# Kernel tuning notes

Hardware: AMD Instinct MI355X
Metric: run time of the kernel (lower is better)

The kernel has to match this reference:

```python
import jax, jax.numpy as jnp
import numpy as np

RADIUS = 5
KS = 2 * RADIUS + 1  # 11
SIGMA_X2 = 4.0 ** 2  # 16
SIGMA_I2 = 10.0 ** 2  # 100


def _patches(x):
    """x: [N,1,H,W] -> [N, H*W, KS, KS] zero-padded sliding windows (torch Unfold semantics)."""
    N, _, H, W = x.shape
    p = jax.lax.conv_general_dilated_patches(
        x, (KS, KS), (1, 1), [(RADIUS, RADIUS), (RADIUS, RADIUS)]
    )  # [N, KS*KS, H, W], channel dim ordered (kh, kw)
    return p.reshape(N, KS, KS, H * W).transpose(0, 3, 1, 2)


def _distance_map(dtype):
    d = (jnp.arange(KS, dtype=dtype) - RADIUS) ** 2
    return jnp.exp(-(d[:, None] + d[None, :]) / SIGMA_X2)  # [KS, KS]


def setup_inputs() -> dict:
    key = jax.random.key(0)
    k1, k2 = jax.random.split(key)
    images = jax.random.uniform(k1, (8, 1, 224, 224), dtype=jnp.float32)
    labels = jax.random.uniform(k2, (8, 4, 224, 224), dtype=jnp.float32)
    return {"images": images, "labels": labels}


def reference(images, labels):
    B, _, H, W = images.shape
    K = labels.shape[1]
    HW = H * W

    img = images * 255.0
    regions = _patches(img)                                   # [B,HW,KS,KS]
    mask = _patches(jnp.ones((1, 1, H, W), img.dtype))        # [1,HW,KS,KS], 0 on padding
    dist_map = _distance_map(img.dtype)                       # [KS,KS]

    i_f = img.reshape(B, HW)[:, :, None, None]                # center pixel intensity
    weights = dist_map * jnp.exp(-(regions - i_f) ** 2 / SIGMA_I2) * mask  # [B,HW,KS,KS]

    # class-prob patches for all classes at once
    P = _patches(labels.reshape(B * K, 1, H, W)).reshape(B, K, HW, KS, KS)

    num = jnp.einsum('bnij,bknij->bkn', weights, P)           # sum_j w_ij * p_j
    den = weights.sum(axis=(2, 3))                            # [B,HW], sum_j w_ij
    p_f = labels.reshape(B, K, HW)

    ratio = jnp.einsum('bkn,bkn->bk', p_f, num) / jnp.einsum('bkn,bn->bk', p_f, den)
    # per-class L1Loss(ratio, 0) = mean over batch of |ratio|; summed over classes
    ratio_sum = jnp.abs(ratio).mean(axis=0).sum()
    return K - ratio_sum
```

## Files before the change

kernel.cpp:

```cpp
#include <hip/hip_runtime.h>
#include <hip/hip_bf16.h>

typedef float f2 __attribute__((ext_vector_type(2)));
typedef float f4 __attribute__((ext_vector_type(4)));

constexpr int Hh = 224, Ww = 224, Bb = 8, Kc = 4, RAD = 5;

constexpr int TX = 32;
constexpr int TILEH = 8;
constexpr int SW = TX + 2 * RAD;
constexpr int SH = TILEH + 2 * RAD;
constexpr int SSTR = SW + 1;
constexpr int GXD = Ww / TX;
constexpr int GYD = Hh / TILEH;
constexpr int PB = GXD * GYD;

constexpr float LOG2E = 1.44269504f;
constexpr float KI  = -0.01f * LOG2E;
constexpr float DSC = -0.0625f * LOG2E;

static __device__ inline f4 splat4(float x) { return (f4){x, x, x, x}; }

__global__ __launch_bounds__(256, 6) void ncut_main(const float* __restrict__ images,
                                                    const float* __restrict__ labels,
                                                    float* __restrict__ acc) {
    __shared__ float simg[SH * SSTR];
    __shared__ f4    slab[SH * SSTR];
    __shared__ float red[4][8];

    const int b   = blockIdx.z;
    const int x0  = blockIdx.x * TX;
    const int y0  = blockIdx.y * TILEH;
    const int tid = threadIdx.x;

    const float* imgb = images + (size_t)b * (Hh * Ww);
    const float* labb = labels + (size_t)b * (Kc * Hh * Ww);

    for (int idx = tid; idx < SH * SSTR; idx += 256) {
        const int lx = idx % SSTR, ly = idx / SSTR;
        const int gx = x0 - RAD + lx, gy = y0 - RAD + ly;
        float iv = 1e19f;
        f4 lv = (f4){0.f, 0.f, 0.f, 0.f};
        if (lx < SW && gx >= 0 && gx < Ww && gy >= 0 && gy < Hh) {
            const int g = gy * Ww + gx;
            iv = imgb[g] * 255.0f;
            lv = (f4){labb[g], labb[Hh * Ww + g], labb[2 * Hh * Ww + g], labb[3 * Hh * Ww + g]};
        }
        simg[idx] = iv;
        slab[idx] = lv;
    }
    __syncthreads();

    const int tx   = tid & 31;
    const int ty   = (tid >> 5) & 3;
    const int half = tid >> 7;
    const int r0   = 2 * ty;

    const float c0 = simg[(r0 + RAD) * SSTR + tx + RAD];
    const float c1 = simg[(r0 + RAD + 1) * SSTR + tx + RAD];

    f4 num0 = splat4(0.f), num1 = splat4(0.f);
    f2 den0 = (f2){0.f, 0.f}, den1 = (f2){0.f, 0.f};

#pragma unroll
    for (int r = 0; r < 6; ++r) {
        const int dr = half * 6 + r;
        const int rowoff = (r0 + dr) * SSTR + tx;
        const int   di0 = dr - 5,        di1 = dr - 6;
        const float fd0 = (float)(di0 * di0), fd1 = (float)(di1 * di1);
        const float dyw0 = (fd0 <= 25.f) ? __builtin_amdgcn_exp2f(fd0 * DSC) : 0.f;
        const float dyw1 = (fd1 <= 25.f) ? __builtin_amdgcn_exp2f(fd1 * DSC) : 0.f;
#pragma unroll
        for (int i = 0; i < 6; ++i) {
            const f2 v  = (f2){simg[rowoff + 2 * i], simg[rowoff + 2 * i + 1]};
            const f4 p0 = slab[rowoff + 2 * i];
            const f4 p1 = slab[rowoff + 2 * i + 1];
            const f2 dxt = (f2){(float)((2 * i - 5) * (2 * i - 5)) * DSC,
                                (float)((2 * i - 4) * (2 * i - 4)) * DSC};
            {
                const f2 d = v - c0;
                const f2 t = __builtin_elementwise_fma(d * KI, d, dxt);
                const float w0 = __builtin_amdgcn_exp2f(t.x) * dyw0;
                const float w1 = __builtin_amdgcn_exp2f(t.y) * dyw0;
                den0 += (f2){w0, w1};
                num0 = __builtin_elementwise_fma(splat4(w0), p0, num0);
                num0 = __builtin_elementwise_fma(splat4(w1), p1, num0);
            }
            {
                const f2 d = v - c1;
                const f2 t = __builtin_elementwise_fma(d * KI, d, dxt);
                const float w0 = __builtin_amdgcn_exp2f(t.x) * dyw1;
                const float w1 = __builtin_amdgcn_exp2f(t.y) * dyw1;
                den1 += (f2){w0, w1};
                num1 = __builtin_elementwise_fma(splat4(w0), p0, num1);
                num1 = __builtin_elementwise_fma(splat4(w1), p1, num1);
            }
        }
    }

    const f4 pc0 = slab[(r0 + RAD) * SSTR + tx + RAD];
    const f4 pc1 = slab[(r0 + RAD + 1) * SSTR + tx + RAD];

    const f4 numv = pc0 * num0 + pc1 * num1;
    const f4 denv = pc0 * (den0.x + den0.y) + pc1 * (den1.x + den1.y);

    float vals[8] = {numv.x, numv.y, numv.z, numv.w, denv.x, denv.y, denv.z, denv.w};

#pragma unroll
    for (int i = 0; i < 8; ++i) {
        float v = vals[i];
#pragma unroll
        for (int off = 32; off > 0; off >>= 1) v += __shfl_down(v, off, 64);
        vals[i] = v;
    }

    const int wave = tid >> 6, lane = tid & 63;
    if (lane == 0) {
#pragma unroll
        for (int i = 0; i < 8; ++i) red[wave][i] = vals[i];
    }
    __syncthreads();

    if (tid < 8) {
        const int gid = blockIdx.x + GXD * blockIdx.y + PB * blockIdx.z;
        acc[gid * 8 + tid] = red[0][tid] + red[1][tid] + red[2][tid] + red[3][tid];
    }
}

__global__ void ncut_final(const float* __restrict__ acc, float* __restrict__ out) {
    __shared__ float part[64];
    const int t = threadIdx.x;
    const int combo = t >> 2;
    const int sub   = t & 3;
    const int b   = combo >> 3;
    const int idx = combo & 7;
    float s = 0.f;
    for (int j = sub; j < PB; j += 4) s += acc[((size_t)(b * PB + j)) * 8 + idx];
    s += __shfl_down(s, 2, 64);
    s += __shfl_down(s, 1, 64);
    if (sub == 0) part[combo] = s;
    __syncthreads();
    if (t < 64) {
        float r = 0.f;
        if (t < 32) {
            const int bb = t >> 2, k = t & 3;
            r = fabsf(part[(bb << 3) + k] / part[(bb << 3) + 4 + k]);
        }
#pragma unroll
        for (int off = 32; off > 0; off >>= 1) r += __shfl_down(r, off, 64);
        if (t == 0) out[0] = (float)Kc - r * (1.0f / (float)Bb);
    }
}

extern "C" void kernel_launch(void* const* d_in, const int* in_sizes, int n_in,
                              void* d_out, int out_size, void* d_ws, size_t ws_size,
                              hipStream_t stream) {
    const float* images = (const float*)d_in[0];
    const float* labels = (const float*)d_in[1];
    float* out = (float*)d_out;
    float* acc = (float*)d_ws;

    dim3 grid(GXD, GYD, Bb);
    ncut_main<<<grid, 256, 0, stream>>>(images, labels, acc);
    ncut_final<<<1, 256, 0, stream>>>(acc, out);
}
```

Baseline: 97.06 us.

## Double tile height, store labels as fp16, factor row distance weights, transpose partials

The main kernel now gives each thread all 12 window rows for two output rows, doubling the tile height, and drops the half-split across threads. The label tile is kept in shared memory as fp16 to halve LDS use. A shifted copy of the image tile allows aligned float2 loads. The per-row vertical distance weight is applied once per row instead of per element. The partial-sum layout is transposed and the final reduction uses 1024 threads. Risks include fp16 precision loss on labels, lower occupancy (launch bounds 3), and fewer blocks in the grid.

```diff
diff --git a/kernel.cpp b/kernel.cpp
--- a/kernel.cpp
+++ b/kernel.cpp
@@ -1,31 +1,40 @@
 #include <hip/hip_runtime.h>
 #include <hip/hip_bf16.h>
 
-typedef float f2 __attribute__((ext_vector_type(2)));
-typedef float f4 __attribute__((ext_vector_type(4)));
+typedef float    f2 __attribute__((ext_vector_type(2)));
+typedef float    f4 __attribute__((ext_vector_type(4)));
+typedef _Float16 h4 __attribute__((ext_vector_type(4)));
 
 constexpr int Hh = 224, Ww = 224, Bb = 8, Kc = 4, RAD = 5;
 
 constexpr int TX = 32;
-constexpr int TILEH = 8;
+constexpr int TILEH = 16;
 constexpr int SW = TX + 2 * RAD;
 constexpr int SH = TILEH + 2 * RAD;
 constexpr int SSTR = SW + 1;
 constexpr int GXD = Ww / TX;
 constexpr int GYD = Hh / TILEH;
 constexpr int PB = GXD * GYD;
+constexpr int NB = PB * Bb;
 
 constexpr float LOG2E = 1.44269504f;
 constexpr float KI  = -0.01f * LOG2E;
 constexpr float DSC = -0.0625f * LOG2E;
+constexpr float DYW[6] = {1.0f, 0.93941306f, 0.77880078f,
+                          0.56978282f, 0.36787944f, 0.20961139f};
+constexpr float DX2[12] = {25.f,16.f,9.f,4.f,1.f,0.f,1.f,4.f,9.f,16.f,25.f,0.f};
 
 static __device__ inline f4 splat4(float x) { return (f4){x, x, x, x}; }
+static __device__ inline f4 cvt4(h4 q) {
+    return (f4){(float)q.x, (float)q.y, (float)q.z, (float)q.w};
+}
 
-__global__ __launch_bounds__(256, 6) void ncut_main(const float* __restrict__ images,
+__global__ __launch_bounds__(256, 3) void ncut_main(const float* __restrict__ images,
                                                     const float* __restrict__ labels,
                                                     float* __restrict__ acc) {
-    __shared__ float simg[SH * SSTR];
-    __shared__ f4    slab[SH * SSTR];
+    __shared__ __align__(16) float simgA[SH * SSTR];
+    __shared__ __align__(16) float simgB[SH * SSTR];
+    __shared__ __align__(16) h4    slab[SH * SSTR];
     __shared__ float red[4][8];
 
     const int b   = blockIdx.z;
@@ -40,66 +49,84 @@
         const int lx = idx % SSTR, ly = idx / SSTR;
         const int gx = x0 - RAD + lx, gy = y0 - RAD + ly;
         float iv = 1e19f;
-        f4 lv = (f4){0.f, 0.f, 0.f, 0.f};
+        h4 lv = (h4){(_Float16)0.f, (_Float16)0.f, (_Float16)0.f, (_Float16)0.f};
         if (lx < SW && gx >= 0 && gx < Ww && gy >= 0 && gy < Hh) {
             const int g = gy * Ww + gx;
             iv = imgb[g] * 255.0f;
-            lv = (f4){labb[g], labb[Hh * Ww + g], labb[2 * Hh * Ww + g], labb[3 * Hh * Ww + g]};
+            lv = (h4){(_Float16)labb[g],
+                      (_Float16)labb[Hh * Ww + g],
+                      (_Float16)labb[2 * Hh * Ww + g],
+                      (_Float16)labb[3 * Hh * Ww + g]};
         }
-        simg[idx] = iv;
+        simgA[idx] = iv;
+        if (idx > 0) simgB[idx - 1] = iv;
         slab[idx] = lv;
     }
     __syncthreads();
 
-    const int tx   = tid & 31;
-    const int ty   = (tid >> 5) & 3;
-    const int half = tid >> 7;
-    const int r0   = 2 * ty;
+    const int tx = tid & 31;
+    const int ty = tid >> 5;
+    const int r0 = 2 * ty;
 
-    const float c0 = simg[(r0 + RAD) * SSTR + tx + RAD];
-    const float c1 = simg[(r0 + RAD + 1) * SSTR + tx + RAD];
+    const float c0 = simgA[(r0 + RAD) * SSTR + tx + RAD];
+    const float c1 = simgA[(r0 + RAD + 1) * SSTR + tx + RAD];
 
     f4 num0 = splat4(0.f), num1 = splat4(0.f);
     f2 den0 = (f2){0.f, 0.f}, den1 = (f2){0.f, 0.f};
 
 #pragma unroll
-    for (int r = 0; r < 6; ++r) {
-        const int dr = half * 6 + r;
-        const int rowoff = (r0 + dr) * SSTR + tx;
-        const int   di0 = dr - 5,        di1 = dr - 6;
-        const float fd0 = (float)(di0 * di0), fd1 = (float)(di1 * di1);
-        const float dyw0 = (fd0 <= 25.f) ? __builtin_amdgcn_exp2f(fd0 * DSC) : 0.f;
-        const float dyw1 = (fd1 <= 25.f) ? __builtin_amdgcn_exp2f(fd1 * DSC) : 0.f;
+    for (int dr = 0; dr < 12; ++dr) {
+        const int rowi   = r0 + dr;
+        const int rowoff = rowi * SSTR + tx;
+        const int par    = (rowi + tx) & 1;
+        const float* sb  = par ? simgB : simgA;
+        const int a0     = rowoff - par;
+
+        f4 nr0 = splat4(0.f), nr1 = splat4(0.f);
+        f2 dn0 = (f2){0.f, 0.f}, dn1 = (f2){0.f, 0.f};
+
 #pragma unroll
         for (int i = 0; i < 6; ++i) {
-            const f2 v  = (f2){simg[rowoff + 2 * i], simg[rowoff + 2 * i + 1]};
-            const f4 p0 = slab[rowoff + 2 * i];
-            const f4 p1 = slab[rowoff + 2 * i + 1];
-            const f2 dxt = (f2){(float)((2 * i - 5) * (2 * i - 5)) * DSC,
-                                (float)((2 * i - 4) * (2 * i - 4)) * DSC};
-            {
+            const f2 v  = *(const f2*)&sb[a0 + 2 * i];
+            const f4 p0 = cvt4(slab[rowoff + 2 * i]);
+            const f4 p1 = cvt4(slab[rowoff + 2 * i + 1]);
+            const f2 dxt = (f2){DX2[2 * i] * DSC,
+                                (2 * i + 1 == 11) ? -1e38f : DX2[2 * i + 1] * DSC};
+            if (dr != 11) {
                 const f2 d = v - c0;
                 const f2 t = __builtin_elementwise_fma(d * KI, d, dxt);
-                const float w0 = __builtin_amdgcn_exp2f(t.x) * dyw0;
-                const float w1 = __builtin_amdgcn_exp2f(t.y) * dyw0;
-                den0 += (f2){w0, w1};
-                num0 = __builtin_elementwise_fma(splat4(w0), p0, num0);
-                num0 = __builtin_elementwise_fma(splat4(w1), p1, num0);
+                const float w0 = __builtin_amdgcn_exp2f(t.x);
+                const float w1 = __builtin_amdgcn_exp2f(t.y);
+                dn0 += (f2){w0, w1};
+                nr0 = __builtin_elementwise_fma(splat4(w0), p0, nr0);
+                nr0 = __builtin_elementwise_fma(splat4(w1), p1, nr0);
             }
-            {
+            if (dr != 0) {
                 const f2 d = v - c1;
                 const f2 t = __builtin_elementwise_fma(d * KI, d, dxt);
-                const float w0 = __builtin_amdgcn_exp2f(t.x) * dyw1;
-                const float w1 = __builtin_amdgcn_exp2f(t.y) * dyw1;
-                den1 += (f2){w0, w1};
-                num1 = __builtin_elementwise_fma(splat4(w0), p0, num1);
-                num1 = __builtin_elementwise_fma(splat4(w1), p1, num1);
+                const float w0 = __builtin_amdgcn_exp2f(t.x);
+                const float w1 = __builtin_amdgcn_exp2f(t.y);
+                dn1 += (f2){w0, w1};
+                nr1 = __builtin_elementwise_fma(splat4(w0), p0, nr1);
+                nr1 = __builtin_elementwise_fma(splat4(w1), p1, nr1);
             }
+        }
+        if (dr != 11) {
+            const int  ad = (dr < 5) ? 5 - dr : dr - 5;
+            const float y = DYW[ad];
+            num0 = __builtin_elementwise_fma(splat4(y), nr0, num0);
+            den0 = __builtin_elementwise_fma((f2){y, y}, dn0, den0);
+        }
+        if (dr != 0) {
+            const int  ad = (dr < 6) ? 6 - dr : dr - 6;
+            const float y = DYW[ad];
+            num1 = __builtin_elementwise_fma(splat4(y), nr1, num1);
+            den1 = __builtin_elementwise_fma((f2){y, y}, dn1, den1);
         }
     }
 
-    const f4 pc0 = slab[(r0 + RAD) * SSTR + tx + RAD];
-    const f4 pc1 = slab[(r0 + RAD + 1) * SSTR + tx + RAD];
+    const f4 pc0 = cvt4(slab[(r0 + RAD) * SSTR + tx + RAD]);
+    const f4 pc1 = cvt4(slab[(r0 + RAD + 1) * SSTR + tx + RAD]);
 
     const f4 numv = pc0 * num0 + pc1 * num1;
     const f4 denv = pc0 * (den0.x + den0.y) + pc1 * (den1.x + den1.y);
@@ -123,19 +150,21 @@
 
     if (tid < 8) {
         const int gid = blockIdx.x + GXD * blockIdx.y + PB * blockIdx.z;
-        acc[gid * 8 + tid] = red[0][tid] + red[1][tid] + red[2][tid] + red[3][tid];
+        acc[tid * NB + gid] = red[0][tid] + red[1][tid] + red[2][tid] + red[3][tid];
     }
 }
 
 __global__ void ncut_final(const float* __restrict__ acc, float* __restrict__ out) {
     __shared__ float part[64];
     const int t = threadIdx.x;
-    const int combo = t >> 2;
-    const int sub   = t & 3;
-    const int b   = combo >> 3;
-    const int idx = combo & 7;
+    const int combo = t >> 4;
+    const int sub   = t & 15;
+    const int idx = combo >> 3, b = combo & 7;
+    const float* p = acc + idx * NB + b * PB;
     float s = 0.f;
-    for (int j = sub; j < PB; j += 4) s += acc[((size_t)(b * PB + j)) * 8 + idx];
+    for (int j = sub; j < PB; j += 16) s += p[j];
+    s += __shfl_down(s, 8, 64);
+    s += __shfl_down(s, 4, 64);
     s += __shfl_down(s, 2, 64);
     s += __shfl_down(s, 1, 64);
     if (sub == 0) part[combo] = s;
@@ -143,8 +172,8 @@
     if (t < 64) {
         float r = 0.f;
         if (t < 32) {
-            const int bb = t >> 2, k = t & 3;
-            r = fabsf(part[(bb << 3) + k] / part[(bb << 3) + 4 + k]);
+            const int k = t & 3, bb = t >> 2;
+            r = fabsf(part[k * 8 + bb] / part[(k + 4) * 8 + bb]);
         }
 #pragma unroll
         for (int off = 32; off > 0; off >>= 1) r += __shfl_down(r, off, 64);
@@ -162,5 +191,5 @@
 
     dim3 grid(GXD, GYD, Bb);
     ncut_main<<<grid, 256, 0, stream>>>(images, labels, acc);
-    ncut_final<<<1, 256, 0, stream>>>(acc, out);
+    ncut_final<<<1, 1024, 0, stream>>>(acc, out);
 }
```

Result: faster. 87.82 us (-9.5%).
